# Performance work log

Measured on AMD Instinct MI355X. Metric: run time of the kernel, lower is better.

## Reference

```python
import jax, jax.numpy as jnp
import numpy as np

B, DIM, HID = 16384, 1024, 64


def setup_inputs() -> dict:
    key = jax.random.key(0)
    k = jax.random.split(key, 6)
    s1 = 1.0 / np.sqrt(2 * DIM)
    s2 = 1.0 / np.sqrt(HID)
    return {
        "q": jax.random.normal(k[0], (B, DIM), jnp.float32),
        "p": jax.random.normal(k[1], (B, DIM), jnp.float32),
        "W1": jax.random.uniform(k[2], (2 * DIM, HID), jnp.float32, -s1, s1),
        "b1": jax.random.uniform(k[3], (HID,), jnp.float32, -s1, s1),
        "W2": jax.random.uniform(k[4], (HID, DIM), jnp.float32, -s2, s2),
        "b2": jax.random.uniform(k[5], (DIM,), jnp.float32, -s2, s2),
        "mass": jnp.ones((DIM,), jnp.float32),
        "dt_param": jnp.float32(0.1),
    }


def _hamiltonian(qp, W1, b1, W2, b2):
    # torch nn.GELU() default is exact (erf) gelu
    h = jax.nn.gelu(qp @ W1 + b1, approximate=False)
    return h @ W2 + b2  # [B, dim]


def reference(q, p, W1, b1, W2, b2, mass, dt_param):
    dim = q.shape[-1]

    def H_sum(qp):
        return _hamiltonian(qp, W1, b1, W2, b2).sum()

    grad_H = jax.grad(H_sum)

    qp = jnp.concatenate([q, p], axis=-1)  # [B, 2*dim]
    g = grad_H(qp)
    dH_dq = g[:, :dim]

    dt = jax.nn.sigmoid(dt_param)
    p_half = p - dt / 2 * dH_dq
    q_new = q + dt / mass[None, :] * p_half

    qp_new = jnp.concatenate([q_new, p_half], axis=-1)
    g2 = grad_H(qp_new)
    dH_dq_new = g2[:, :dim]
    p_new = p_half - dt / 2 * dH_dq_new

    energy_conserved = jnp.abs(
        _hamiltonian(qp, W1, b1, W2, b2)
        - _hamiltonian(jnp.concatenate([q_new, p_new], axis=-1), W1, b1, W2, b2)
    )  # [B, dim]
    return q_new, p_new, energy_conserved
```

## Files before the change

kernel.cpp:

```cpp
#include <hip/hip_runtime.h>
#include <stdint.h>

#define BROWS 16384
#define DIMN 1024
#define HIDN 64

typedef __attribute__((ext_vector_type(8))) short bf16x8;
typedef __attribute__((ext_vector_type(4))) float f32x4;

__device__ __forceinline__ unsigned short f2bf(float f) {
    union { float f; unsigned int u; } v; v.f = f;
    unsigned int u = v.u;
    u += 0x7fffu + ((u >> 16) & 1u);
    return (unsigned short)(u >> 16);
}

__device__ __forceinline__ bf16x8 pack8(float4 a, float4 b) {
    bf16x8 r;
    r[0] = (short)f2bf(a.x); r[1] = (short)f2bf(a.y);
    r[2] = (short)f2bf(a.z); r[3] = (short)f2bf(a.w);
    r[4] = (short)f2bf(b.x); r[5] = (short)f2bf(b.y);
    r[6] = (short)f2bf(b.z); r[7] = (short)f2bf(b.w);
    return r;
}

__device__ __forceinline__ float geluf(float x) {
    return 0.5f * x * (1.0f + erff(x * 0.70710678118654752f));
}
__device__ __forceinline__ float dgeluf(float x) {
    float c = 0.5f * (1.0f + erff(x * 0.70710678118654752f));
    return c + x * 0.3989422804014327f * expf(-0.5f * x * x);
}


__global__ void prep_kernel(const float* __restrict__ W1, const float* __restrict__ W2,
                            const float* __restrict__ mass, const float* __restrict__ dtp,
                            unsigned short* __restrict__ W1bf,
                            unsigned short* __restrict__ W1Tbf,
                            unsigned short* __restrict__ W2Tbf,
                            unsigned short* __restrict__ W1qdT,
                            float* __restrict__ dtm, float* __restrict__ w2sum) {
    if (blockIdx.x == 0) {
        __shared__ float partw[4][64];
        int k = threadIdx.x & 63, c = threadIdx.x >> 6;
        float s = 0.f;
        const float* row = W2 + (size_t)k * DIMN + c * 256;
        #pragma unroll 8
        for (int j = 0; j < 256; ++j) s += row[j];
        partw[c][k] = s;
        __syncthreads();
        if (c == 0) w2sum[k] = partw[0][k] + partw[1][k] + partw[2][k] + partw[3][k];
    }
    int gid = blockIdx.x * blockDim.x + threadIdx.x;
    int nt = gridDim.x * blockDim.x;
    float dt = 1.0f / (1.0f + expf(-dtp[0]));
    for (int i = gid; i < 2048 * 64; i += nt) {
        unsigned short b = f2bf(W1[i]);
        W1bf[i] = b;
        int k = i >> 6, n = i & 63;
        W1Tbf[n * 2048 + k] = b;
    }
    for (int i = gid; i < 64 * 1024; i += nt) {
        int k = i >> 10, n = i & 1023;
        W2Tbf[n * 64 + k] = f2bf(W2[i]);
    }
    for (int i = gid; i < 64 * 1024; i += nt) {
        int n = i >> 10, k = i & 1023;
        W1qdT[i] = f2bf((dt / mass[k]) * W1[k * 64 + n]);
    }
    for (int i = gid; i < DIMN; i += nt) dtm[i] = dt / mass[i];
}


__global__ __launch_bounds__(256)
void mnkern(const unsigned short* __restrict__ W1T, const unsigned short* __restrict__ W1qdT,
            float* __restrict__ MN, float* __restrict__ Nm) {
    const int wv = threadIdx.x >> 6, lane = threadIdx.x & 63;
    const int l16 = lane & 15, quad = lane >> 4, kq = quad * 8;
    const int gw = blockIdx.x * 4 + wv;
    const int mt = gw >> 2, nt = gw & 3;
    f32x4 accMd = {0,0,0,0}, accN = {0,0,0,0};
    #pragma unroll 4
    for (int it = 0; it < 32; ++it) {
        int k = it * 32 + kq;
        bf16x8 af = *(const bf16x8*)(W1T + (size_t)(mt * 16 + l16) * 2048 + k);
        bf16x8 bd = *(const bf16x8*)(W1qdT + (size_t)(nt * 16 + l16) * 1024 + k);
        bf16x8 bp = *(const bf16x8*)(W1T + (size_t)(nt * 16 + l16) * 2048 + 1024 + k);
        accMd = __builtin_amdgcn_mfma_f32_16x16x32_bf16(af, bd, accMd, 0, 0, 0);
        accN  = __builtin_amdgcn_mfma_f32_16x16x32_bf16(af, bp, accN, 0, 0, 0);
    }
    #pragma unroll
    for (int rg = 0; rg < 4; ++rg) {
        int row = mt * 16 + quad * 4 + rg;
        int col = nt * 16 + l16;
        MN[row * 64 + col] = accMd[rg] + accN[rg];
        Nm[row * 64 + col] = accN[rg];
    }
}


__global__ __launch_bounds__(256, 4)
void zchain(const float* __restrict__ q, const float* __restrict__ p,
            const unsigned short* __restrict__ W1T, const unsigned short* __restrict__ W1qdT,
            const float* __restrict__ b1,
            const float* __restrict__ MN, const float* __restrict__ Nm,
            const float* __restrict__ w2sum, const float* __restrict__ dtp,
            unsigned short* __restrict__ u1b, unsigned short* __restrict__ usb,
            unsigned short* __restrict__ g13) {
    __shared__ float part[4 * 64 * 34];
    __shared__ float ubuf[4 * 256];
    const int wv = threadIdx.x >> 6, lane = threadIdx.x & 63;
    const int l16 = lane & 15, quad = lane >> 4, kq = quad * 8;
    const int tile = blockIdx.x;
    const size_t arow = (size_t)tile * 16 + l16;
    const float* rq = q + arow * DIMN + wv * 256;
    const float* rp = p + arow * DIMN + wv * 256;

    f32x4 accz[4] = {{0,0,0,0},{0,0,0,0},{0,0,0,0},{0,0,0,0}};
    f32x4 accd[4] = {{0,0,0,0},{0,0,0,0},{0,0,0,0},{0,0,0,0}};

    float4 cq0 = *(const float4*)(rq + kq);
    float4 cq1 = *(const float4*)(rq + kq + 4);
    float4 cp0 = *(const float4*)(rp + kq);
    float4 cp1 = *(const float4*)(rp + kq + 4);
    #pragma unroll
    for (int it = 0; it < 8; ++it) {
        float4 nq0 = {0,0,0,0}, nq1 = {0,0,0,0}, np0 = {0,0,0,0}, np1 = {0,0,0,0};
        if (it < 7) {
            int kn = (it + 1) * 32 + kq;
            nq0 = *(const float4*)(rq + kn); nq1 = *(const float4*)(rq + kn + 4);
            np0 = *(const float4*)(rp + kn); np1 = *(const float4*)(rp + kn + 4);
        }
        const int k = wv * 256 + it * 32 + kq;
        bf16x8 aq = pack8(cq0, cq1);
        bf16x8 ap = pack8(cp0, cp1);
        #pragma unroll
        for (int c = 0; c < 4; ++c) {
            bf16x8 bq = *(const bf16x8*)(W1T + (size_t)(c * 16 + l16) * 2048 + k);
            accz[c] = __builtin_amdgcn_mfma_f32_16x16x32_bf16(aq, bq, accz[c], 0, 0, 0);
        }
        #pragma unroll
        for (int c = 0; c < 4; ++c) {
            bf16x8 bp = *(const bf16x8*)(W1T + (size_t)(c * 16 + l16) * 2048 + 1024 + k);
            accz[c] = __builtin_amdgcn_mfma_f32_16x16x32_bf16(ap, bp, accz[c], 0, 0, 0);
            bf16x8 bd = *(const bf16x8*)(W1qdT + (size_t)(c * 16 + l16) * 1024 + k);
            accd[c] = __builtin_amdgcn_mfma_f32_16x16x32_bf16(ap, bd, accd[c], 0, 0, 0);
        }
        cq0 = nq0; cq1 = nq1; cp0 = np0; cp1 = np1;
    }

    float* myp = part + (size_t)(wv * 64 + lane) * 34;
    #pragma unroll
    for (int c = 0; c < 4; ++c) {
        #pragma unroll
        for (int rg = 0; rg < 4; ++rg) {
            myp[c * 4 + rg] = accz[c][rg];
            myp[16 + c * 4 + rg] = accd[c][rg];
        }
    }
    __syncthreads();

    float z1v[4], zdv[4];
    #pragma unroll
    for (int kk = 0; kk < 4; ++kk) {
        const int row = wv + kk * 4, col = lane;
        const int ln = ((row >> 2) << 4) | (col & 15);
        const int j = ((col >> 4) << 2) | (row & 3);
        float sz = b1[col], sd = 0.f;
        #pragma unroll
        for (int w = 0; w < 4; ++w) {
            const float* pp = part + (size_t)(w * 64 + ln) * 34;
            sz += pp[j];
            sd += pp[16 + j];
        }
        z1v[kk] = sz;
        zdv[kk] = sd;
    }

    float* ub = ubuf + wv * 256;
    const float ws = w2sum[lane];
    const float hdt = 0.5f / (1.0f + expf(-dtp[0]));

    float u1[4], h1[4];
    #pragma unroll
    for (int r = 0; r < 4; ++r) {
        u1[r] = dgeluf(z1v[r]) * ws;
        h1[r] = geluf(z1v[r]);
        ub[r * 64 + lane] = u1[r];
    }
    float acc[4] = {0.f, 0.f, 0.f, 0.f};
    #pragma unroll 8
    for (int k = 0; k < 64; ++k) {
        float m = MN[k * 64 + lane];
        acc[0] += ub[k] * m;
        acc[1] += ub[64 + k] * m;
        acc[2] += ub[128 + k] * m;
        acc[3] += ub[192 + k] * m;
    }
    float z2[4], u2[4];
    #pragma unroll
    for (int r = 0; r < 4; ++r) {
        z2[r] = z1v[r] + zdv[r] - hdt * acc[r];
        u2[r] = dgeluf(z2[r]) * ws;
        ub[r * 64 + lane] = u2[r];
    }
    float acc2[4] = {0.f, 0.f, 0.f, 0.f};
    #pragma unroll 8
    for (int k = 0; k < 64; ++k) {
        float m = Nm[k * 64 + lane];
        acc2[0] += ub[k] * m;
        acc2[1] += ub[64 + k] * m;
        acc2[2] += ub[128 + k] * m;
        acc2[3] += ub[192 + k] * m;
    }
    #pragma unroll
    for (int r = 0; r < 4; ++r) {
        float z3 = z2[r] - hdt * acc2[r];
        size_t o = ((size_t)tile * 16 + wv + r * 4) * 64 + lane;
        u1b[o] = f2bf(u1[r]);
        usb[o] = f2bf(u1[r] + u2[r]);
        g13[o] = f2bf(h1[r] - geluf(z3));
    }
}


__global__ __launch_bounds__(256, 4)
void wide4(const unsigned short* __restrict__ u1b, const unsigned short* __restrict__ usb,
           const unsigned short* __restrict__ g13,
           const unsigned short* __restrict__ W1bf, const unsigned short* __restrict__ W2T,
           const float* __restrict__ q, const float* __restrict__ p,
           const float* __restrict__ dtm, const float* __restrict__ dtp,
           float* __restrict__ outq, float* __restrict__ outp, float* __restrict__ oute) {
    const int wv = threadIdx.x >> 6, lane = threadIdx.x & 63;
    const int l16 = lane & 15, quad = lane >> 4, kq = quad * 8;
    const int gw = blockIdx.x * 4 + wv;
    const int mt = gw >> 4;
    const int ng = (gw & 15) * 4;
    const size_t arow = (size_t)mt * 16 + l16;

    bf16x8 au0 = *(const bf16x8*)(u1b + arow * 64 + kq);
    bf16x8 au1 = *(const bf16x8*)(u1b + arow * 64 + 32 + kq);
    bf16x8 as0 = *(const bf16x8*)(usb + arow * 64 + kq);
    bf16x8 as1 = *(const bf16x8*)(usb + arow * 64 + 32 + kq);
    bf16x8 ag0 = *(const bf16x8*)(g13 + arow * 64 + kq);
    bf16x8 ag1 = *(const bf16x8*)(g13 + arow * 64 + 32 + kq);

    const float hdt = 0.5f / (1.0f + expf(-dtp[0]));

    #pragma unroll
    for (int t = 0; t < 4; ++t) {
        const int n0 = (ng + t) * 16;
        bf16x8 bw0 = *(const bf16x8*)(W1bf + (size_t)(n0 + l16) * 64 + kq);
        bf16x8 bw1 = *(const bf16x8*)(W1bf + (size_t)(n0 + l16) * 64 + 32 + kq);
        bf16x8 b20 = *(const bf16x8*)(W2T + (size_t)(n0 + l16) * 64 + kq);
        bf16x8 b21 = *(const bf16x8*)(W2T + (size_t)(n0 + l16) * 64 + 32 + kq);

        f32x4 accq = {0,0,0,0}, accs = {0,0,0,0}, acce = {0,0,0,0};
        accq = __builtin_amdgcn_mfma_f32_16x16x32_bf16(au0, bw0, accq, 0, 0, 0);
        accq = __builtin_amdgcn_mfma_f32_16x16x32_bf16(au1, bw1, accq, 0, 0, 0);
        accs = __builtin_amdgcn_mfma_f32_16x16x32_bf16(as0, bw0, accs, 0, 0, 0);
        accs = __builtin_amdgcn_mfma_f32_16x16x32_bf16(as1, bw1, accs, 0, 0, 0);
        acce = __builtin_amdgcn_mfma_f32_16x16x32_bf16(ag0, b20, acce, 0, 0, 0);
        acce = __builtin_amdgcn_mfma_f32_16x16x32_bf16(ag1, b21, acce, 0, 0, 0);

        const int i = n0 + l16;
        const float dm = dtm[i];
        #pragma unroll
        for (int rg = 0; rg < 4; ++rg) {
            size_t idx = (size_t)(mt * 16 + quad * 4 + rg) * DIMN + i;
            float qv = q[idx], pv = p[idx];
            float ph = pv - hdt * accq[rg];
            outq[idx] = qv + dm * ph;
            outp[idx] = pv - hdt * accs[rg];
            oute[idx] = fabsf(acce[rg]);
        }
    }
}


extern "C" void kernel_launch(void* const* d_in, const int* in_sizes, int n_in,
                              void* d_out, int out_size, void* d_ws, size_t ws_size,
                              hipStream_t stream) {
    const float* q    = (const float*)d_in[0];
    const float* p    = (const float*)d_in[1];
    const float* W1   = (const float*)d_in[2];
    const float* b1   = (const float*)d_in[3];
    const float* W2   = (const float*)d_in[4];
    const float* mass = (const float*)d_in[6];
    const float* dtp  = (const float*)d_in[7];

    float* out  = (float*)d_out;
    float* outq = out;
    float* outp = out + (size_t)BROWS * DIMN;
    float* oute = out + (size_t)2 * BROWS * DIMN;

    char* ws = (char*)d_ws;
    unsigned short* W1bf  = (unsigned short*)(ws);
    unsigned short* W1Tbf = (unsigned short*)(ws + 262144);
    unsigned short* W2Tbf = (unsigned short*)(ws + 524288);
    float* w2sum          = (float*)(ws + 655360);
    float* dtm            = (float*)(ws + 655616);
    unsigned short* W1qdT = (unsigned short*)(ws + 659712);
    float* MN             = (float*)(ws + 790784);
    float* Nm             = (float*)(ws + 807168);
    unsigned short* u1b   = (unsigned short*)(ws + 9437184);
    unsigned short* usb   = (unsigned short*)(ws + 11534336);
    unsigned short* g13   = (unsigned short*)(ws + 13631488);

    hipLaunchKernelGGL(prep_kernel, dim3(256), dim3(256), 0, stream,
                       W1, W2, mass, dtp, W1bf, W1Tbf, W2Tbf, W1qdT, dtm, w2sum);
    hipLaunchKernelGGL(mnkern, dim3(4), dim3(256), 0, stream, W1Tbf, W1qdT, MN, Nm);
    hipLaunchKernelGGL(zchain, dim3(1024), dim3(256), 0, stream,
                       q, p, W1Tbf, W1qdT, b1, MN, Nm, w2sum, dtp, u1b, usb, g13);
    hipLaunchKernelGGL(wide4, dim3(4096), dim3(256), 0, stream,
                       u1b, usb, g13, W1bf, W2Tbf, q, p, dtm, dtp, outq, outp, oute);
}
```

Baseline: 428.5 us.

## Fuse zchain and wide4 into one kernel with LDS-staged bf16 intermediates

Merges the per-tile hidden-state chain and the wide output GEMM into a single kernel. The u1/us/g13 bf16 intermediates are staged in LDS, reusing the partial-sum buffer, instead of making a global round trip. Each block now handles all 1024 output columns for its 16 rows across 4 waves with 16 iterations each, and outputs are written with nontemporal stores. This removes one launch and the intermediate traffic, at the cost of fewer blocks (1024 vs 4096) and a longer serial output loop per wave, which may reduce latency hiding.

After: 417.1 us. 2.7% less time.

```diff
diff --git a/kernel.cpp b/kernel.cpp
--- a/kernel.cpp
+++ b/kernel.cpp
@@ -100,15 +100,15 @@
 
 
 __global__ __launch_bounds__(256, 4)
-void zchain(const float* __restrict__ q, const float* __restrict__ p,
-            const unsigned short* __restrict__ W1T, const unsigned short* __restrict__ W1qdT,
-            const float* __restrict__ b1,
-            const float* __restrict__ MN, const float* __restrict__ Nm,
-            const float* __restrict__ w2sum, const float* __restrict__ dtp,
-            unsigned short* __restrict__ u1b, unsigned short* __restrict__ usb,
-            unsigned short* __restrict__ g13) {
+void megakern(const float* __restrict__ q, const float* __restrict__ p,
+              const unsigned short* __restrict__ W1T, const unsigned short* __restrict__ W1qdT,
+              const unsigned short* __restrict__ W1bf, const unsigned short* __restrict__ W2T,
+              const float* __restrict__ b1,
+              const float* __restrict__ MN, const float* __restrict__ Nm,
+              const float* __restrict__ w2sum, const float* __restrict__ dtm,
+              const float* __restrict__ dtp,
+              float* __restrict__ outq, float* __restrict__ outp, float* __restrict__ oute) {
     __shared__ float part[4 * 64 * 34];
-    __shared__ float ubuf[4 * 256];
     const int wv = threadIdx.x >> 6, lane = threadIdx.x & 63;
     const int l16 = lane & 15, quad = lane >> 4, kq = quad * 8;
     const int tile = blockIdx.x;
@@ -163,10 +163,9 @@
     float z1v[4], zdv[4];
     #pragma unroll
     for (int kk = 0; kk < 4; ++kk) {
-        const int row = wv + kk * 4, col = lane;
-        const int ln = ((row >> 2) << 4) | (col & 15);
-        const int j = ((col >> 4) << 2) | (row & 3);
-        float sz = b1[col], sd = 0.f;
+        const int ln = (kk << 4) | l16;
+        const int j = (quad << 2) | wv;
+        float sz = b1[lane], sd = 0.f;
         #pragma unroll
         for (int w = 0; w < 4; ++w) {
             const float* pp = part + (size_t)(w * 64 + ln) * 34;
@@ -176,8 +175,14 @@
         z1v[kk] = sz;
         zdv[kk] = sd;
     }
-
-    float* ub = ubuf + wv * 256;
+    __syncthreads();
+
+    float* ub = part + wv * 256;
+    unsigned short* ubf16 = (unsigned short*)(part + 1024);
+    unsigned short* u1lds = ubf16;
+    unsigned short* uslds = ubf16 + 16 * 72;
+    unsigned short* g13lds = ubf16 + 2 * 16 * 72;
+
     const float ws = w2sum[lane];
     const float hdt = 0.5f / (1.0f + expf(-dtp[0]));
 
@@ -216,40 +221,23 @@
     #pragma unroll
     for (int r = 0; r < 4; ++r) {
         float z3 = z2[r] - hdt * acc2[r];
-        size_t o = ((size_t)tile * 16 + wv + r * 4) * 64 + lane;
-        u1b[o] = f2bf(u1[r]);
-        usb[o] = f2bf(u1[r] + u2[r]);
-        g13[o] = f2bf(h1[r] - geluf(z3));
-    }
-}
-
-
-__global__ __launch_bounds__(256, 4)
-void wide4(const unsigned short* __restrict__ u1b, const unsigned short* __restrict__ usb,
-           const unsigned short* __restrict__ g13,
-           const unsigned short* __restrict__ W1bf, const unsigned short* __restrict__ W2T,
-           const float* __restrict__ q, const float* __restrict__ p,
-           const float* __restrict__ dtm, const float* __restrict__ dtp,
-           float* __restrict__ outq, float* __restrict__ outp, float* __restrict__ oute) {
-    const int wv = threadIdx.x >> 6, lane = threadIdx.x & 63;
-    const int l16 = lane & 15, quad = lane >> 4, kq = quad * 8;
-    const int gw = blockIdx.x * 4 + wv;
-    const int mt = gw >> 4;
-    const int ng = (gw & 15) * 4;
-    const size_t arow = (size_t)mt * 16 + l16;
-
-    bf16x8 au0 = *(const bf16x8*)(u1b + arow * 64 + kq);
-    bf16x8 au1 = *(const bf16x8*)(u1b + arow * 64 + 32 + kq);
-    bf16x8 as0 = *(const bf16x8*)(usb + arow * 64 + kq);
-    bf16x8 as1 = *(const bf16x8*)(usb + arow * 64 + 32 + kq);
-    bf16x8 ag0 = *(const bf16x8*)(g13 + arow * 64 + kq);
-    bf16x8 ag1 = *(const bf16x8*)(g13 + arow * 64 + 32 + kq);
-
-    const float hdt = 0.5f / (1.0f + expf(-dtp[0]));
-
-    #pragma unroll
-    for (int t = 0; t < 4; ++t) {
-        const int n0 = (ng + t) * 16;
+        const int row = wv + r * 4;
+        u1lds[row * 72 + lane] = f2bf(u1[r]);
+        uslds[row * 72 + lane] = f2bf(u1[r] + u2[r]);
+        g13lds[row * 72 + lane] = f2bf(h1[r] - geluf(z3));
+    }
+    __syncthreads();
+
+    const bf16x8 au0 = *(const bf16x8*)(u1lds + l16 * 72 + kq);
+    const bf16x8 au1 = *(const bf16x8*)(u1lds + l16 * 72 + 32 + kq);
+    const bf16x8 as0 = *(const bf16x8*)(uslds + l16 * 72 + kq);
+    const bf16x8 as1 = *(const bf16x8*)(uslds + l16 * 72 + 32 + kq);
+    const bf16x8 ag0 = *(const bf16x8*)(g13lds + l16 * 72 + kq);
+    const bf16x8 ag1 = *(const bf16x8*)(g13lds + l16 * 72 + 32 + kq);
+
+    #pragma unroll 2
+    for (int t = 0; t < 16; ++t) {
+        const int n0 = (wv * 16 + t) * 16;
         bf16x8 bw0 = *(const bf16x8*)(W1bf + (size_t)(n0 + l16) * 64 + kq);
         bf16x8 bw1 = *(const bf16x8*)(W1bf + (size_t)(n0 + l16) * 64 + 32 + kq);
         bf16x8 b20 = *(const bf16x8*)(W2T + (size_t)(n0 + l16) * 64 + kq);
@@ -267,12 +255,12 @@
         const float dm = dtm[i];
         #pragma unroll
         for (int rg = 0; rg < 4; ++rg) {
-            size_t idx = (size_t)(mt * 16 + quad * 4 + rg) * DIMN + i;
+            size_t idx = (size_t)(tile * 16 + quad * 4 + rg) * DIMN + i;
             float qv = q[idx], pv = p[idx];
             float ph = pv - hdt * accq[rg];
-            outq[idx] = qv + dm * ph;
-            outp[idx] = pv - hdt * accs[rg];
-            oute[idx] = fabsf(acce[rg]);
+            __builtin_nontemporal_store(qv + dm * ph, &outq[idx]);
+            __builtin_nontemporal_store(pv - hdt * accs[rg], &outp[idx]);
+            __builtin_nontemporal_store(fabsf(acce[rg]), &oute[idx]);
         }
     }
 }
@@ -303,15 +291,11 @@
     unsigned short* W1qdT = (unsigned short*)(ws + 659712);
     float* MN             = (float*)(ws + 790784);
     float* Nm             = (float*)(ws + 807168);
-    unsigned short* u1b   = (unsigned short*)(ws + 9437184);
-    unsigned short* usb   = (unsigned short*)(ws + 11534336);
-    unsigned short* g13   = (unsigned short*)(ws + 13631488);
 
     hipLaunchKernelGGL(prep_kernel, dim3(256), dim3(256), 0, stream,
                        W1, W2, mass, dtp, W1bf, W1Tbf, W2Tbf, W1qdT, dtm, w2sum);
     hipLaunchKernelGGL(mnkern, dim3(4), dim3(256), 0, stream, W1Tbf, W1qdT, MN, Nm);
-    hipLaunchKernelGGL(zchain, dim3(1024), dim3(256), 0, stream,
-                       q, p, W1Tbf, W1qdT, b1, MN, Nm, w2sum, dtp, u1b, usb, g13);
-    hipLaunchKernelGGL(wide4, dim3(4096), dim3(256), 0, stream,
-                       u1b, usb, g13, W1bf, W2Tbf, q, p, dtm, dtp, outq, outp, oute);
-}
+    hipLaunchKernelGGL(megakern, dim3(1024), dim3(256), 0, stream,
+                       q, p, W1Tbf, W1qdT, W1bf, W2Tbf, b1, MN, Nm,
+                       w2sum, dtm, dtp, outq, outp, oute);
+}
```
